# Kernel tuning notes

Measured on AMD Instinct MI355X. Metric: run time of the kernel, lower is better.

The kernel has to match this reference:

```python
import jax, jax.numpy as jnp
import numpy as np

BN_EPS = 1e-5


def _square_distance(src, dst):
    # src: (B,N,3), dst: (B,S,3) -> (B,N,S) squared euclidean distance
    d = -2.0 * jnp.einsum('bnc,bsc->bns', src, dst)
    d += jnp.sum(src * src, -1)[:, :, None]
    d += jnp.sum(dst * dst, -1)[:, None, :]
    return d


def _bn_relu(x, gamma, beta):
    # training-mode BatchNorm1d over (B, C, N): stats over (B, N)
    mean = jnp.mean(x, axis=(0, 2), keepdims=True)
    var = jnp.var(x, axis=(0, 2), keepdims=True)  # biased, as torch uses for normalization
    xhat = (x - mean) * jax.lax.rsqrt(var + BN_EPS)
    return jax.nn.relu(xhat * gamma[None, :, None] + beta[None, :, None])


def setup_inputs() -> dict:
    key = jax.random.key(0)
    ks = jax.random.split(key, 8)
    B, N, S, C1, C2 = 4, 8192, 2048, 128, 256
    inp = {
        'xyz1': jax.random.normal(ks[0], (B, 3, N), jnp.float32),
        'xyz2': jax.random.normal(ks[1], (B, 3, S), jnp.float32),
        'points1': jax.random.normal(ks[2], (B, C1, N), jnp.float32),
        'points2': jax.random.normal(ks[3], (B, C2, S), jnp.float32),
        'w0': jax.random.normal(ks[4], (256, C1 + C2), jnp.float32) * (1.0 / np.sqrt(C1 + C2)),
        'b0': jnp.zeros((256,), jnp.float32),
        'gamma0': jnp.ones((256,), jnp.float32),
        'beta0': jnp.zeros((256,), jnp.float32),
        'w1': jax.random.normal(ks[5], (128, 256), jnp.float32) * (1.0 / np.sqrt(256)),
        'b1': jnp.zeros((128,), jnp.float32),
        'gamma1': jnp.ones((128,), jnp.float32),
        'beta1': jnp.zeros((128,), jnp.float32),
    }
    return inp


def reference(xyz1, xyz2, points1, points2, w0, b0, gamma0, beta0, w1, b1, gamma1, beta1):
    B, _, N = xyz1.shape
    S = xyz2.shape[2]
    xyz1_t = jnp.transpose(xyz1, (0, 2, 1))  # (B,N,3)
    xyz2_t = jnp.transpose(xyz2, (0, 2, 1))  # (B,S,3)
    dist = _square_distance(xyz1_t, xyz2_t)  # (B,N,S)
    neg_d3, idx = jax.lax.top_k(-dist, 3)    # 3 smallest distances
    d3 = -neg_d3                             # (B,N,3)
    dist_recip = 1.0 / (d3 + 1e-8)
    weight = dist_recip / jnp.sum(dist_recip, axis=2, keepdims=True)  # (B,N,3)
    points2_t = jnp.transpose(points2, (0, 2, 1))  # (B,S,C2)
    bidx = jnp.arange(B)[:, None, None]
    neighbor = points2_t[bidx, idx]                 # (B,N,3,C2)
    interp = jnp.sum(neighbor * weight[..., None], axis=2)  # (B,N,C2)
    interp = jnp.transpose(interp, (0, 2, 1))               # (B,C2,N)
    x = jnp.concatenate([points1, interp], axis=1)          # (B,C1+C2,N)
    x = _bn_relu(jnp.einsum('oc,bcn->bon', w0, x) + b0[None, :, None], gamma0, beta0)
    x = _bn_relu(jnp.einsum('oc,bcn->bon', w1, x) + b1[None, :, None], gamma1, beta1)
    return x
```

## Files before the change

kernel.cpp:

```cpp
#include <hip/hip_runtime.h>
#include <hip/hip_bf16.h>

#define BATCH 4
#define NPTS  8192
#define SPTS  2048
#define C1    128
#define C2    256
#define CIN   384
#define H0    256
#define H1    128
#define NTOTF 32768.0f
#define NPART 512

typedef __attribute__((ext_vector_type(8))) short bf16x8;
typedef __attribute__((ext_vector_type(4))) float f32x4;

__device__ __forceinline__ unsigned short f2bf(float x) {
  union { float f; unsigned u; } v; v.f = x;
  unsigned r = v.u + 0x7fff + ((v.u >> 16) & 1);
  return (unsigned short)(r >> 16);
}
__device__ __forceinline__ float bf2f(unsigned short u) {
  union { unsigned u; float f; } v; v.u = ((unsigned)u) << 16; return v.f;
}

__global__ __launch_bounds__(256) void prep_kernel(
    const float* __restrict__ p2, unsigned short* __restrict__ p2tb,
    const float* __restrict__ xyz2, float4* __restrict__ xp,
    const float* __restrict__ w0, const float* __restrict__ w1,
    unsigned short* __restrict__ Wp,
    const float* __restrict__ p1, unsigned short* __restrict__ Xp) {
  __shared__ unsigned short shmem[64 * 136];
  int bid = blockIdx.x;
  int t = threadIdx.x;

  if (bid < 512) {
    int b = bid >> 7, rem = bid & 127;
    int s0 = (rem >> 2) * 64, c0 = (rem & 3) * 64;
    const float* src = p2 + (size_t)b * C2 * SPTS;
    int ss = t & 63, cseg = t >> 6;
#pragma unroll
    for (int i = 0; i < 16; i++) {
      int cc = cseg + i * 4;
      shmem[ss * 72 + cc] = f2bf(src[(size_t)(c0 + cc) * SPTS + s0 + ss]);
    }
    __syncthreads();
    int s = t >> 2, chunk = t & 3;
    uint4 v0 = *(const uint4*)&shmem[s * 72 + chunk * 16];
    uint4 v1 = *(const uint4*)&shmem[s * 72 + chunk * 16 + 8];
    unsigned short* dst = p2tb + (size_t)b * SPTS * C2 + (size_t)(s0 + s) * C2 + c0 + chunk * 16;
    *(uint4*)dst = v0;
    *(uint4*)(dst + 8) = v1;
  } else if (bid < 1024) {
    int b2 = bid - 512;
    int b = b2 >> 7, n0 = (b2 & 127) * 64;
    int nn = t & 63, c4 = t >> 6;
#pragma unroll
    for (int i = 0; i < 32; i++) {
      int c = i * 4 + c4;
      shmem[nn * 136 + c] = f2bf(p1[((size_t)b * C1 + c) * NPTS + n0 + nn]);
    }
    __syncthreads();
    int n = t >> 2;
#pragma unroll
    for (int j = 0; j < 4; j++) {
      int ch = (t & 3) + j * 4;
      uint4 v = *(const uint4*)&shmem[n * 136 + ch * 8];
      *(uint4*)&Xp[((size_t)b * NPTS + n0 + n) * CIN + ch * 8] = v;
    }
  } else if (bid < 1056) {
    int idx = (bid - 1024) * 256 + t;
    int b = idx >> 11, s = idx & (SPTS - 1);
    const float* x2 = xyz2 + (size_t)b * 3 * SPTS;
    float x = x2[s], y = x2[SPTS + s], z = x2[2 * SPTS + s];
    xp[idx] = make_float4(x, y, z, x * x + y * y + z * z);
  } else {
    int idx = ((bid - 1056) * 256 + t) * 4;
    const float* src = (idx < H0 * CIN) ? (w0 + idx) : (w1 + (idx - H0 * CIN));
    float4 v = *(const float4*)src;
    ushort4 o;
    o.x = f2bf(v.x); o.y = f2bf(v.y); o.z = f2bf(v.z); o.w = f2bf(v.w);
    *(ushort4*)(Wp + idx) = o;
  }
}

#define INS3(d, s, e0, e1, e2, j0, j1, j2)                        \
  {                                                               \
    bool lt0 = (d) < (e0), lt1 = (d) < (e1), lt2 = (d) < (e2);    \
    j2 = lt1 ? (j1) : (lt2 ? (s) : (j2));                         \
    j1 = lt0 ? (j0) : (lt1 ? (s) : (j1));                         \
    j0 = lt0 ? (s) : (j0);                                        \
    e2 = __builtin_amdgcn_fmed3f((d), (e1), (e2));                \
    e1 = __builtin_amdgcn_fmed3f((d), (e0), (e1));                \
    e0 = fminf((d), (e0));                                        \
  }

__global__ __launch_bounds__(1024) void knn_kernel(
    const float* __restrict__ xyz1, const float4* __restrict__ xp,
    int* __restrict__ nidx, float* __restrict__ nw) {
  int b = blockIdx.y;
  int t = threadIdx.x;
  int lane = t & 63;
  int w = __builtin_amdgcn_readfirstlane(t >> 6);
  int n = blockIdx.x * 64 + lane;
  const float* x1 = xyz1 + (size_t)b * 3 * NPTS;
  float px = x1[n], py = x1[NPTS + n], pz = x1[2 * NPTS + n];

  const int CHUNK = SPTS / 16;
  int sbase = w * CHUNK;
  const float4* cp = xp + (size_t)b * SPTS + sbase;

  float d0 = 3e38f, d1 = 3e38f, d2 = 3e38f;
  int i0 = 0, i1 = 0, i2 = 0;
#pragma unroll 8
  for (int j = 0; j < CHUNK; j++) {
    float4 c = cp[j];
    float qc = fmaf(py, c.y, px * c.x);
    qc = fmaf(pz, c.z, qc);
    float d = fmaf(-2.f, qc, c.w);
    int s = sbase + j;
    INS3(d, s, d0, d1, d2, i0, i1, i2);
  }

  __shared__ float dsh[16][64][3];
  __shared__ int   ish[16][64][3];
  dsh[w][lane][0] = d0; dsh[w][lane][1] = d1; dsh[w][lane][2] = d2;
  ish[w][lane][0] = i0; ish[w][lane][1] = i1; ish[w][lane][2] = i2;
  __syncthreads();

  if (t < 256) {
    int g = t >> 6, q = t & 63;
    float e0 = 3e38f, e1 = 3e38f, e2 = 3e38f;
    int j0 = 0, j1 = 0, j2 = 0;
#pragma unroll
    for (int c = 0; c < 4; c++) {
#pragma unroll
      for (int k = 0; k < 3; k++) {
        float d = dsh[4 * g + c][q][k];
        int s = ish[4 * g + c][q][k];
        INS3(d, s, e0, e1, e2, j0, j1, j2);
      }
    }
    dsh[4 * g][q][0] = e0; dsh[4 * g][q][1] = e1; dsh[4 * g][q][2] = e2;
    ish[4 * g][q][0] = j0; ish[4 * g][q][1] = j1; ish[4 * g][q][2] = j2;
  }
  __syncthreads();

  if (t < 64) {
    float e0 = 3e38f, e1 = 3e38f, e2 = 3e38f;
    int j0 = 0, j1 = 0, j2 = 0;
#pragma unroll
    for (int c = 0; c < 4; c++) {
#pragma unroll
      for (int k = 0; k < 3; k++) {
        float d = dsh[4 * c][t][k];
        int s = ish[4 * c][t][k];
        INS3(d, s, e0, e1, e2, j0, j1, j2);
      }
    }
    float qq = px * px + py * py + pz * pz;
    float r0 = 1.f / (e0 + qq + 1e-8f);
    float r1 = 1.f / (e1 + qq + 1e-8f);
    float r2 = 1.f / (e2 + qq + 1e-8f);
    float rs = 1.f / (r0 + r1 + r2);
    int base = (b * NPTS + n) * 3;
    nidx[base + 0] = j0; nidx[base + 1] = j1; nidx[base + 2] = j2;
    nw[base + 0] = r0 * rs; nw[base + 1] = r1 * rs; nw[base + 2] = r2 * rs;
  }
}

__global__ __launch_bounds__(256) void interp_kernel(
    const unsigned short* __restrict__ p2tb, const int* __restrict__ nidx,
    const float* __restrict__ nw, unsigned short* __restrict__ Xp) {
  const int PTS = 8;
  int bid = blockIdx.x;
  int b = bid / (NPTS / PTS);
  int p0 = (bid % (NPTS / PTS)) * PTS;
  int c = threadIdx.x;
  const unsigned short* base = p2tb + (size_t)b * SPTS * C2;
#pragma unroll
  for (int k = 0; k < PTS; k++) {
    int p = p0 + k;
    int ib = (b * NPTS + p) * 3;
    int i0 = nidx[ib], i1 = nidx[ib + 1], i2 = nidx[ib + 2];
    float w0v = nw[ib], w1v = nw[ib + 1], w2v = nw[ib + 2];
    float v = w0v * bf2f(base[(size_t)i0 * C2 + c]) +
              w1v * bf2f(base[(size_t)i1 * C2 + c]) +
              w2v * bf2f(base[(size_t)i2 * C2 + c]);
    Xp[((size_t)b * NPTS + p) * CIN + C1 + c] = f2bf(v);
  }
}

__global__ __launch_bounds__(256) void gemm1_kernel(
    const unsigned short* __restrict__ A, const unsigned short* __restrict__ X,
    const float* __restrict__ bias, unsigned short* __restrict__ X1,
    float* __restrict__ gp0s, float* __restrict__ gp0q) {
  __shared__ unsigned short As[128 * 32];
  __shared__ unsigned short Bs[128 * 32];
  int b = blockIdx.z;
  int n0 = blockIdx.x * 128;
  int o0 = blockIdx.y * 128;
  int t = threadIdx.x;
  int lane = t & 63;
  int w = __builtin_amdgcn_readfirstlane(t >> 6);
  int mhalf = (w & 1) * 64, nhalf = (w >> 1) * 64;
  const unsigned short* Xb = X + (size_t)b * NPTS * CIN;

  f32x4 acc[4][4] = {};
  int rA = lane >> 2;
  int cofs = (lane & 3) * 8;

  for (int k0 = 0; k0 < CIN; k0 += 32) {
#pragma unroll
    for (int q = 0; q < 2; q++) {
      int r0 = w * 32 + q * 16;
      const unsigned short* ga = A + (size_t)(o0 + r0 + rA) * CIN + k0 + cofs;
      __builtin_amdgcn_global_load_lds(
          (const __attribute__((address_space(1))) void*)ga,
          (__attribute__((address_space(3))) void*)(As + r0 * 32), 16, 0, 0);
      const unsigned short* gb = Xb + (size_t)(n0 + r0 + rA) * CIN + k0 + cofs;
      __builtin_amdgcn_global_load_lds(
          (const __attribute__((address_space(1))) void*)gb,
          (__attribute__((address_space(3))) void*)(Bs + r0 * 32), 16, 0, 0);
    }
    __syncthreads();

    bf16x8 af[4], bfr[4];
    int mi = lane & 15, kq = (lane >> 4) * 8;
#pragma unroll
    for (int i = 0; i < 4; i++) {
      af[i]  = *(const bf16x8*)(As + (mhalf + i * 16 + mi) * 32 + kq);
      bfr[i] = *(const bf16x8*)(Bs + (nhalf + i * 16 + mi) * 32 + kq);
    }
#pragma unroll
    for (int mt = 0; mt < 4; mt++)
#pragma unroll
      for (int nt = 0; nt < 4; nt++)
        acc[mt][nt] = __builtin_amdgcn_mfma_f32_16x16x32_bf16(
            af[mt], bfr[nt], acc[mt][nt], 0, 0, 0);
    __syncthreads();
  }

  int mi = lane & 15;
  int rq = (lane >> 4) * 4;
  unsigned short* Xo = X1 + (size_t)b * NPTS * H0;
  int pidx = (b * 64 + blockIdx.x) * 2 + (w >> 1);
#pragma unroll
  for (int mt = 0; mt < 4; mt++) {
    int mbase = o0 + mhalf + mt * 16 + rq;
    float4 bv = *(const float4*)&bias[mbase];
    float sv[4] = {0.f, 0.f, 0.f, 0.f}, sq[4] = {0.f, 0.f, 0.f, 0.f};
#pragma unroll
    for (int nt = 0; nt < 4; nt++) {
      int n = n0 + nhalf + nt * 16 + mi;
      float v0 = acc[mt][nt][0] + bv.x;
      float v1 = acc[mt][nt][1] + bv.y;
      float v2 = acc[mt][nt][2] + bv.z;
      float v3 = acc[mt][nt][3] + bv.w;
      ushort4 o;
      o.x = f2bf(v0); o.y = f2bf(v1); o.z = f2bf(v2); o.w = f2bf(v3);
      *(ushort4*)&Xo[(size_t)n * H0 + mbase] = o;
      sv[0] += v0; sq[0] += v0 * v0;
      sv[1] += v1; sq[1] += v1 * v1;
      sv[2] += v2; sq[2] += v2 * v2;
      sv[3] += v3; sq[3] += v3 * v3;
    }
#pragma unroll
    for (int r = 0; r < 4; r++) {
#pragma unroll
      for (int msk = 1; msk < 16; msk <<= 1) {
        sv[r] += __shfl_xor(sv[r], msk);
        sq[r] += __shfl_xor(sq[r], msk);
      }
    }
    if (mi == 0) {
#pragma unroll
      for (int r = 0; r < 4; r++) {
        gp0s[(size_t)(mbase + r) * NPART + pidx] = sv[r];
        gp0q[(size_t)(mbase + r) * NPART + pidx] = sq[r];
      }
    }
  }
}

template <int C>
__global__ __launch_bounds__(64) void fin_kernel(
    const float* __restrict__ gs, const float* __restrict__ gq,
    const float* __restrict__ gamma, const float* __restrict__ beta,
    float* __restrict__ a, float* __restrict__ s) {
  int ch = blockIdx.x * 64 + threadIdx.x;
  const float4* ps = (const float4*)(gs + (size_t)ch * NPART);
  const float4* pq = (const float4*)(gq + (size_t)ch * NPART);
  float sum = 0.f, sq = 0.f;
  for (int p = 0; p < NPART / 4; p++) {
    float4 v = ps[p]; sum += v.x + v.y + v.z + v.w;
    float4 u = pq[p]; sq += u.x + u.y + u.z + u.w;
  }
  const float inv = 1.f / NTOTF;
  float mean = sum * inv;
  float var = sq * inv - mean * mean;
  float ia = gamma[ch] * rsqrtf(var + 1e-5f);
  a[ch] = ia;
  s[ch] = beta[ch] - mean * ia;
}

__global__ __launch_bounds__(256) void bnrelu_kernel(
    unsigned short* __restrict__ X1, const float* __restrict__ a,
    const float* __restrict__ s) {
  size_t base = ((size_t)blockIdx.x * 256 + threadIdx.x) * 8;
  int c = (int)(base & (H0 - 1));
  float4 a0 = *(const float4*)&a[c];
  float4 a1 = *(const float4*)&a[c + 4];
  float4 s0 = *(const float4*)&s[c];
  float4 s1 = *(const float4*)&s[c + 4];
  ushort4 x0 = *(ushort4*)&X1[base];
  ushort4 x1 = *(ushort4*)&X1[base + 4];
  ushort4 o0, o1;
  o0.x = f2bf(fmaxf(bf2f(x0.x) * a0.x + s0.x, 0.f));
  o0.y = f2bf(fmaxf(bf2f(x0.y) * a0.y + s0.y, 0.f));
  o0.z = f2bf(fmaxf(bf2f(x0.z) * a0.z + s0.z, 0.f));
  o0.w = f2bf(fmaxf(bf2f(x0.w) * a0.w + s0.w, 0.f));
  o1.x = f2bf(fmaxf(bf2f(x1.x) * a1.x + s1.x, 0.f));
  o1.y = f2bf(fmaxf(bf2f(x1.y) * a1.y + s1.y, 0.f));
  o1.z = f2bf(fmaxf(bf2f(x1.z) * a1.z + s1.z, 0.f));
  o1.w = f2bf(fmaxf(bf2f(x1.w) * a1.w + s1.w, 0.f));
  *(ushort4*)&X1[base] = o0;
  *(ushort4*)&X1[base + 4] = o1;
}

__global__ __launch_bounds__(256) void gemm2_kernel(
    const unsigned short* __restrict__ A, const unsigned short* __restrict__ X,
    const float* __restrict__ bias, float* __restrict__ Y,
    float* __restrict__ gp1s, float* __restrict__ gp1q) {
  __shared__ unsigned short As[128 * 32];
  __shared__ unsigned short Bs[128 * 32];
  int b = blockIdx.z;
  int n0 = blockIdx.x * 128;
  int t = threadIdx.x;
  int lane = t & 63;
  int w = __builtin_amdgcn_readfirstlane(t >> 6);
  int mhalf = (w & 1) * 64, nhalf = (w >> 1) * 64;
  const unsigned short* Xb = X + (size_t)b * NPTS * H0;

  f32x4 acc[4][4] = {};
  int rA = lane >> 2;
  int cofs = (lane & 3) * 8;

  for (int k0 = 0; k0 < H0; k0 += 32) {
#pragma unroll
    for (int q = 0; q < 2; q++) {
      int r0 = w * 32 + q * 16;
      const unsigned short* ga = A + (size_t)(r0 + rA) * H0 + k0 + cofs;
      __builtin_amdgcn_global_load_lds(
          (const __attribute__((address_space(1))) void*)ga,
          (__attribute__((address_space(3))) void*)(As + r0 * 32), 16, 0, 0);
      const unsigned short* gb = Xb + (size_t)(n0 + r0 + rA) * H0 + k0 + cofs;
      __builtin_amdgcn_global_load_lds(
          (const __attribute__((address_space(1))) void*)gb,
          (__attribute__((address_space(3))) void*)(Bs + r0 * 32), 16, 0, 0);
    }
    __syncthreads();

    bf16x8 af[4], bfr[4];
    int mi = lane & 15, kq = (lane >> 4) * 8;
#pragma unroll
    for (int i = 0; i < 4; i++) {
      af[i]  = *(const bf16x8*)(As + (mhalf + i * 16 + mi) * 32 + kq);
      bfr[i] = *(const bf16x8*)(Bs + (nhalf + i * 16 + mi) * 32 + kq);
    }
#pragma unroll
    for (int mt = 0; mt < 4; mt++)
#pragma unroll
      for (int nt = 0; nt < 4; nt++)
        acc[mt][nt] = __builtin_amdgcn_mfma_f32_16x16x32_bf16(
            af[mt], bfr[nt], acc[mt][nt], 0, 0, 0);
    __syncthreads();
  }

  int mi = lane & 15;
  int rq = (lane >> 4) * 4;
  float* Yb = Y + (size_t)b * H1 * NPTS;
  int pidx = (b * 64 + blockIdx.x) * 2 + (w >> 1);
#pragma unroll
  for (int mt = 0; mt < 4; mt++) {
    int mbase = mhalf + mt * 16 + rq;
    float4 bv = *(const float4*)&bias[mbase];
    float sv[4] = {0.f, 0.f, 0.f, 0.f}, sq[4] = {0.f, 0.f, 0.f, 0.f};
#pragma unroll
    for (int nt = 0; nt < 4; nt++) {
      int n = n0 + nhalf + nt * 16 + mi;
      float v0 = acc[mt][nt][0] + bv.x;
      float v1 = acc[mt][nt][1] + bv.y;
      float v2 = acc[mt][nt][2] + bv.z;
      float v3 = acc[mt][nt][3] + bv.w;
      Yb[(size_t)(mbase + 0) * NPTS + n] = v0;
      Yb[(size_t)(mbase + 1) * NPTS + n] = v1;
      Yb[(size_t)(mbase + 2) * NPTS + n] = v2;
      Yb[(size_t)(mbase + 3) * NPTS + n] = v3;
      sv[0] += v0; sq[0] += v0 * v0;
      sv[1] += v1; sq[1] += v1 * v1;
      sv[2] += v2; sq[2] += v2 * v2;
      sv[3] += v3; sq[3] += v3 * v3;
    }
#pragma unroll
    for (int r = 0; r < 4; r++) {
#pragma unroll
      for (int msk = 1; msk < 16; msk <<= 1) {
        sv[r] += __shfl_xor(sv[r], msk);
        sq[r] += __shfl_xor(sq[r], msk);
      }
    }
    if (mi == 0) {
#pragma unroll
      for (int r = 0; r < 4; r++) {
        gp1s[(size_t)(mbase + r) * NPART + pidx] = sv[r];
        gp1q[(size_t)(mbase + r) * NPART + pidx] = sq[r];
      }
    }
  }
}

__global__ __launch_bounds__(256) void bn_apply_kernel(
    float* __restrict__ Y, const float* __restrict__ a, const float* __restrict__ s) {
  int idx = blockIdx.x * 256 + threadIdx.x;
  int i = idx * 4;
  int c = (i >> 13) & (H1 - 1);
  float ia = a[c], sh = s[c];
  float4 v = *(float4*)(Y + i);
  v.x = fmaxf(v.x * ia + sh, 0.f);
  v.y = fmaxf(v.y * ia + sh, 0.f);
  v.z = fmaxf(v.z * ia + sh, 0.f);
  v.w = fmaxf(v.w * ia + sh, 0.f);
  *(float4*)(Y + i) = v;
}

extern "C" void kernel_launch(void* const* d_in, const int* in_sizes, int n_in,
                              void* d_out, int out_size, void* d_ws, size_t ws_size,
                              hipStream_t stream) {
  const float* xyz1    = (const float*)d_in[0];
  const float* xyz2    = (const float*)d_in[1];
  const float* points1 = (const float*)d_in[2];
  const float* points2 = (const float*)d_in[3];
  const float* w0      = (const float*)d_in[4];
  const float* b0      = (const float*)d_in[5];
  const float* gamma0  = (const float*)d_in[6];
  const float* beta0   = (const float*)d_in[7];
  const float* w1      = (const float*)d_in[8];
  const float* b1      = (const float*)d_in[9];
  const float* gamma1  = (const float*)d_in[10];
  const float* beta1   = (const float*)d_in[11];
  float* out = (float*)d_out;

  char* ws = (char*)d_ws;
  unsigned short* p2tb = (unsigned short*)ws;  ws += (size_t)BATCH * SPTS * C2 * 2;
  unsigned short* Xp = (unsigned short*)ws;    ws += (size_t)BATCH * NPTS * CIN * 2;
  unsigned short* X1 = (unsigned short*)ws;    ws += (size_t)BATCH * NPTS * H0 * 2;
  unsigned short* Wp = (unsigned short*)ws;    ws += (size_t)(H0 * CIN + H1 * H0) * 2;
  int* nidx = (int*)ws;                        ws += (size_t)BATCH * NPTS * 3 * 4;
  float* nw = (float*)ws;                      ws += (size_t)BATCH * NPTS * 3 * 4;
  float4* xyz2p = (float4*)(((uintptr_t)ws + 15) & ~(uintptr_t)15);
  ws = (char*)xyz2p + (size_t)BATCH * SPTS * 16;
  float* gp0s = (float*)ws;                    ws += (size_t)H0 * NPART * 4;
  float* gp0q = (float*)ws;                    ws += (size_t)H0 * NPART * 4;
  float* gp1s = (float*)ws;                    ws += (size_t)H1 * NPART * 4;
  float* gp1q = (float*)ws;                    ws += (size_t)H1 * NPART * 4;
  float* a0 = (float*)ws;                      ws += 1024;
  float* s0 = (float*)ws;                      ws += 1024;
  float* a1 = (float*)ws;                      ws += 1024;
  float* s1 = (float*)ws;                      ws += 1024;
  (void)ws_size; (void)in_sizes; (void)n_in; (void)out_size;

  prep_kernel<<<dim3(1184), 256, 0, stream>>>(points2, p2tb, xyz2, xyz2p,
                                              w0, w1, Wp, points1, Xp);
  knn_kernel<<<dim3(NPTS / 64, BATCH), 1024, 0, stream>>>(xyz1, xyz2p, nidx, nw);
  interp_kernel<<<dim3(BATCH * NPTS / 8), 256, 0, stream>>>(p2tb, nidx, nw, Xp);

  gemm1_kernel<<<dim3(NPTS / 128, H0 / 128, BATCH), 256, 0, stream>>>(
      Wp, Xp, b0, X1, gp0s, gp0q);
  fin_kernel<H0><<<dim3(H0 / 64), 64, 0, stream>>>(gp0s, gp0q, gamma0, beta0, a0, s0);
  bnrelu_kernel<<<dim3((int)((size_t)BATCH * NPTS * H0 / 2048)), 256, 0, stream>>>(X1, a0, s0);
  gemm2_kernel<<<dim3(NPTS / 128, 1, BATCH), 256, 0, stream>>>(
      Wp + H0 * CIN, X1, b1, out, gp1s, gp1q);
  fin_kernel<H1><<<dim3(H1 / 64), 64, 0, stream>>>(gp1s, gp1q, gamma1, beta1, a1, s1);
  bn_apply_kernel<<<dim3(BATCH * H1 * NPTS / 1024), 256, 0, stream>>>(out, a1, s1);
}
```

Before: 203.7 us.

## Write GEMM1 output channel-major and compute BN0 stats in separate pass

GEMM1 no longer reduces BatchNorm partial sums in its epilogue. It writes a channel-major bf16 intermediate with scalar 2-byte stores. A new per-channel kernel rereads that buffer to compute mean and variance from bf16-rounded values. A tiled apply kernel then transposes back to point-major while applying BN+ReLU. This moves the stats reduction out of the GEMM epilogue at the cost of an extra buffer, an extra full read pass, narrow strided stores, and statistics computed from rounded values.

```diff
diff --git a/kernel.cpp b/kernel.cpp
--- a/kernel.cpp
+++ b/kernel.cpp
@@ -193,8 +193,7 @@
 
 __global__ __launch_bounds__(256) void gemm1_kernel(
     const unsigned short* __restrict__ A, const unsigned short* __restrict__ X,
-    const float* __restrict__ bias, unsigned short* __restrict__ X1,
-    float* __restrict__ gp0s, float* __restrict__ gp0q) {
+    const float* __restrict__ bias, unsigned short* __restrict__ Y0) {
   __shared__ unsigned short As[128 * 32];
   __shared__ unsigned short Bs[128 * 32];
   int b = blockIdx.z;
@@ -243,89 +242,77 @@
 
   int mi = lane & 15;
   int rq = (lane >> 4) * 4;
-  unsigned short* Xo = X1 + (size_t)b * NPTS * H0;
-  int pidx = (b * 64 + blockIdx.x) * 2 + (w >> 1);
+  unsigned short* Yb = Y0 + (size_t)b * H0 * NPTS;
 #pragma unroll
   for (int mt = 0; mt < 4; mt++) {
-    int mbase = o0 + mhalf + mt * 16 + rq;
-    float4 bv = *(const float4*)&bias[mbase];
-    float sv[4] = {0.f, 0.f, 0.f, 0.f}, sq[4] = {0.f, 0.f, 0.f, 0.f};
-#pragma unroll
-    for (int nt = 0; nt < 4; nt++) {
-      int n = n0 + nhalf + nt * 16 + mi;
-      float v0 = acc[mt][nt][0] + bv.x;
-      float v1 = acc[mt][nt][1] + bv.y;
-      float v2 = acc[mt][nt][2] + bv.z;
-      float v3 = acc[mt][nt][3] + bv.w;
-      ushort4 o;
-      o.x = f2bf(v0); o.y = f2bf(v1); o.z = f2bf(v2); o.w = f2bf(v3);
-      *(ushort4*)&Xo[(size_t)n * H0 + mbase] = o;
-      sv[0] += v0; sq[0] += v0 * v0;
-      sv[1] += v1; sq[1] += v1 * v1;
-      sv[2] += v2; sq[2] += v2 * v2;
-      sv[3] += v3; sq[3] += v3 * v3;
-    }
 #pragma unroll
     for (int r = 0; r < 4; r++) {
-#pragma unroll
-      for (int msk = 1; msk < 16; msk <<= 1) {
-        sv[r] += __shfl_xor(sv[r], msk);
-        sq[r] += __shfl_xor(sq[r], msk);
+      int m = o0 + mhalf + mt * 16 + rq + r;
+      float bv = bias[m];
+#pragma unroll
+      for (int nt = 0; nt < 4; nt++) {
+        int n = n0 + nhalf + nt * 16 + mi;
+        Yb[(size_t)m * NPTS + n] = f2bf(acc[mt][nt][r] + bv);
       }
     }
-    if (mi == 0) {
-#pragma unroll
-      for (int r = 0; r < 4; r++) {
-        gp0s[(size_t)(mbase + r) * NPART + pidx] = sv[r];
-        gp0q[(size_t)(mbase + r) * NPART + pidx] = sq[r];
-      }
-    }
   }
 }
 
 template <int C>
-__global__ __launch_bounds__(64) void fin_kernel(
-    const float* __restrict__ gs, const float* __restrict__ gq,
-    const float* __restrict__ gamma, const float* __restrict__ beta,
-    float* __restrict__ a, float* __restrict__ s) {
-  int ch = blockIdx.x * 64 + threadIdx.x;
-  const float4* ps = (const float4*)(gs + (size_t)ch * NPART);
-  const float4* pq = (const float4*)(gq + (size_t)ch * NPART);
+__global__ __launch_bounds__(256) void bn_stats_bf16_kernel(
+    const unsigned short* __restrict__ Y, const float* __restrict__ gamma,
+    const float* __restrict__ beta, float* __restrict__ a, float* __restrict__ s) {
+  int o = blockIdx.x;
+  int t = threadIdx.x;
   float sum = 0.f, sq = 0.f;
-  for (int p = 0; p < NPART / 4; p++) {
-    float4 v = ps[p]; sum += v.x + v.y + v.z + v.w;
-    float4 u = pq[p]; sq += u.x + u.y + u.z + u.w;
-  }
-  const float inv = 1.f / NTOTF;
-  float mean = sum * inv;
-  float var = sq * inv - mean * mean;
-  float ia = gamma[ch] * rsqrtf(var + 1e-5f);
-  a[ch] = ia;
-  s[ch] = beta[ch] - mean * ia;
-}
-
-__global__ __launch_bounds__(256) void bnrelu_kernel(
-    unsigned short* __restrict__ X1, const float* __restrict__ a,
-    const float* __restrict__ s) {
-  size_t base = ((size_t)blockIdx.x * 256 + threadIdx.x) * 8;
-  int c = (int)(base & (H0 - 1));
-  float4 a0 = *(const float4*)&a[c];
-  float4 a1 = *(const float4*)&a[c + 4];
-  float4 s0 = *(const float4*)&s[c];
-  float4 s1 = *(const float4*)&s[c + 4];
-  ushort4 x0 = *(ushort4*)&X1[base];
-  ushort4 x1 = *(ushort4*)&X1[base + 4];
-  ushort4 o0, o1;
-  o0.x = f2bf(fmaxf(bf2f(x0.x) * a0.x + s0.x, 0.f));
-  o0.y = f2bf(fmaxf(bf2f(x0.y) * a0.y + s0.y, 0.f));
-  o0.z = f2bf(fmaxf(bf2f(x0.z) * a0.z + s0.z, 0.f));
-  o0.w = f2bf(fmaxf(bf2f(x0.w) * a0.w + s0.w, 0.f));
-  o1.x = f2bf(fmaxf(bf2f(x1.x) * a1.x + s1.x, 0.f));
-  o1.y = f2bf(fmaxf(bf2f(x1.y) * a1.y + s1.y, 0.f));
-  o1.z = f2bf(fmaxf(bf2f(x1.z) * a1.z + s1.z, 0.f));
-  o1.w = f2bf(fmaxf(bf2f(x1.w) * a1.w + s1.w, 0.f));
-  *(ushort4*)&X1[base] = o0;
-  *(ushort4*)&X1[base + 4] = o1;
+  for (int b = 0; b < BATCH; b++) {
+    const unsigned short* p = Y + ((size_t)b * C + o) * NPTS;
+    for (int n = t * 4; n < NPTS; n += 1024) {
+      ushort4 v = *(const ushort4*)(p + n);
+      float x0 = bf2f(v.x), x1 = bf2f(v.y), x2 = bf2f(v.z), x3 = bf2f(v.w);
+      sum += x0 + x1 + x2 + x3;
+      sq += x0 * x0 + x1 * x1 + x2 * x2 + x3 * x3;
+    }
+  }
+  __shared__ float r1[256], r2[256];
+  r1[t] = sum; r2[t] = sq;
+  __syncthreads();
+  for (int off = 128; off > 0; off >>= 1) {
+    if (t < off) { r1[t] += r1[t + off]; r2[t] += r2[t + off]; }
+    __syncthreads();
+  }
+  if (t == 0) {
+    float inv = 1.f / NTOTF;
+    float mean = r1[0] * inv;
+    float var = r2[0] * inv - mean * mean;
+    float ia = gamma[o] * rsqrtf(var + 1e-5f);
+    a[o] = ia;
+    s[o] = beta[o] - mean * ia;
+  }
+}
+
+__global__ __launch_bounds__(256) void bn0_apply_kernel(
+    const unsigned short* __restrict__ Y0, const float* __restrict__ a,
+    const float* __restrict__ s, unsigned short* __restrict__ X1) {
+  __shared__ unsigned short tile[64][80];
+  int b = blockIdx.z, o0 = blockIdx.y * 64, n0 = blockIdx.x * 64;
+  int t = threadIdx.x;
+  int nn = t & 63, o4 = t >> 6;
+#pragma unroll
+  for (int i = 0; i < 16; i++) {
+    int o = i * 4 + o4;
+    float v = bf2f(Y0[((size_t)b * H0 + o0 + o) * NPTS + n0 + nn]);
+    v = fmaxf(v * a[o0 + o] + s[o0 + o], 0.f);
+    tile[nn][o] = f2bf(v);
+  }
+  __syncthreads();
+  int n = t >> 2;
+#pragma unroll
+  for (int j = 0; j < 2; j++) {
+    int ch = (t & 3) + j * 4;
+    uint4 v = *(const uint4*)&tile[n][ch * 8];
+    *(uint4*)&X1[((size_t)b * NPTS + n0 + n) * H0 + o0 + ch * 8] = v;
+  }
 }
 
 __global__ __launch_bounds__(256) void gemm2_kernel(
@@ -418,6 +405,26 @@
       }
     }
   }
+}
+
+__global__ __launch_bounds__(64) void fin_kernel(
+    const float* __restrict__ gs, const float* __restrict__ gq,
+    const float* __restrict__ gamma, const float* __restrict__ beta,
+    float* __restrict__ a, float* __restrict__ s) {
+  int ch = blockIdx.x * 64 + threadIdx.x;
+  const float4* ps = (const float4*)(gs + (size_t)ch * NPART);
+  const float4* pq = (const float4*)(gq + (size_t)ch * NPART);
+  float sum = 0.f, sq = 0.f;
+  for (int p = 0; p < NPART / 4; p++) {
+    float4 v = ps[p]; sum += v.x + v.y + v.z + v.w;
+    float4 u = pq[p]; sq += u.x + u.y + u.z + u.w;
+  }
+  const float inv = 1.f / NTOTF;
+  float mean = sum * inv;
+  float var = sq * inv - mean * mean;
+  float ia = gamma[ch] * rsqrtf(var + 1e-5f);
+  a[ch] = ia;
+  s[ch] = beta[ch] - mean * ia;
 }
 
 __global__ __launch_bounds__(256) void bn_apply_kernel(
@@ -454,14 +461,13 @@
   char* ws = (char*)d_ws;
   unsigned short* p2tb = (unsigned short*)ws;  ws += (size_t)BATCH * SPTS * C2 * 2;
   unsigned short* Xp = (unsigned short*)ws;    ws += (size_t)BATCH * NPTS * CIN * 2;
+  unsigned short* Y0 = (unsigned short*)ws;    ws += (size_t)BATCH * H0 * NPTS * 2;
   unsigned short* X1 = (unsigned short*)ws;    ws += (size_t)BATCH * NPTS * H0 * 2;
   unsigned short* Wp = (unsigned short*)ws;    ws += (size_t)(H0 * CIN + H1 * H0) * 2;
   int* nidx = (int*)ws;                        ws += (size_t)BATCH * NPTS * 3 * 4;
   float* nw = (float*)ws;                      ws += (size_t)BATCH * NPTS * 3 * 4;
   float4* xyz2p = (float4*)(((uintptr_t)ws + 15) & ~(uintptr_t)15);
   ws = (char*)xyz2p + (size_t)BATCH * SPTS * 16;
-  float* gp0s = (float*)ws;                    ws += (size_t)H0 * NPART * 4;
-  float* gp0q = (float*)ws;                    ws += (size_t)H0 * NPART * 4;
   float* gp1s = (float*)ws;                    ws += (size_t)H1 * NPART * 4;
   float* gp1q = (float*)ws;                    ws += (size_t)H1 * NPART * 4;
   float* a0 = (float*)ws;                      ws += 1024;
@@ -475,12 +481,11 @@
   knn_kernel<<<dim3(NPTS / 64, BATCH), 1024, 0, stream>>>(xyz1, xyz2p, nidx, nw);
   interp_kernel<<<dim3(BATCH * NPTS / 8), 256, 0, stream>>>(p2tb, nidx, nw, Xp);
 
-  gemm1_kernel<<<dim3(NPTS / 128, H0 / 128, BATCH), 256, 0, stream>>>(
-      Wp, Xp, b0, X1, gp0s, gp0q);
-  fin_kernel<H0><<<dim3(H0 / 64), 64, 0, stream>>>(gp0s, gp0q, gamma0, beta0, a0, s0);
-  bnrelu_kernel<<<dim3((int)((size_t)BATCH * NPTS * H0 / 2048)), 256, 0, stream>>>(X1, a0, s0);
+  gemm1_kernel<<<dim3(NPTS / 128, H0 / 128, BATCH), 256, 0, stream>>>(Wp, Xp, b0, Y0);
+  bn_stats_bf16_kernel<H0><<<H0, 256, 0, stream>>>(Y0, gamma0, beta0, a0, s0);
+  bn0_apply_kernel<<<dim3(NPTS / 64, H0 / 64, BATCH), 256, 0, stream>>>(Y0, a0, s0, X1);
   gemm2_kernel<<<dim3(NPTS / 128, 1, BATCH), 256, 0, stream>>>(
       Wp + H0 * CIN, X1, b1, out, gp1s, gp1q);
-  fin_kernel<H1><<<dim3(H1 / 64), 64, 0, stream>>>(gp1s, gp1q, gamma1, beta1, a1, s1);
+  fin_kernel<<<dim3(H1 / 64), 64, 0, stream>>>(gp1s, gp1q, gamma1, beta1, a1, s1);
   bn_apply_kernel<<<dim3(BATCH * H1 * NPTS / 1024), 256, 0, stream>>>(out, a1, s1);
 }
```

Result: faster. 198.5 us (-2.6%).
